# Performance work log

Measured on AMD Instinct MI355X. Metric: run time of the kernel, lower is better.

## Reference

```python
import jax, jax.numpy as jnp
import numpy as np

B, S, V, D, H, L = 2, 1024, 32000, 1024, 16, 4
DK = D // H
DF = 4 * D
EPS = 1e-5


def setup_inputs() -> dict:
    key = jax.random.key(0)
    ks = jax.random.split(key, 9)
    s = 0.02
    rn = lambda k, shape: jax.random.normal(k, shape, jnp.float32) * s
    return {
        "input_ids": jax.random.randint(ks[0], (B, S), 0, V, dtype=jnp.int32),
        "emb": rn(ks[1], (V, D)),
        "Wq": rn(ks[2], (L, D, D)),
        "Wk": rn(ks[3], (L, D, D)),
        "Wv": rn(ks[4], (L, D, D)),
        "Wo": rn(ks[5], (L, D, D)),
        "W1": rn(ks[6], (L, D, DF)),
        "b1": jnp.zeros((L, DF), jnp.float32),
        "W2": rn(ks[7], (L, DF, D)),
        "b2": jnp.zeros((L, D), jnp.float32),
        "ln1_g": jnp.ones((L, D), jnp.float32),
        "ln1_b": jnp.zeros((L, D), jnp.float32),
        "ln2_g": jnp.ones((L, D), jnp.float32),
        "ln2_b": jnp.zeros((L, D), jnp.float32),
        "lnf_g": jnp.ones((D,), jnp.float32),
        "lnf_b": jnp.zeros((D,), jnp.float32),
        "head_w": rn(ks[8], (D, V)),
    }


def _ln(x, g, b):
    m = jnp.mean(x, -1, keepdims=True)
    v = jnp.mean(jnp.square(x - m), -1, keepdims=True)
    return (x - m) * jax.lax.rsqrt(v + EPS) * g + b


def _heads(x):
    # [B,S,D] -> [B,H,S,DK]
    return x.reshape(B, S, H, DK).transpose(0, 2, 1, 3)


def _forward(input_ids, emb, Wq, Wk, Wv, Wo, W1, b1, W2, b2,
             ln1_g, ln1_b, ln2_g, ln2_b, lnf_g, lnf_b, head_w):
    x = emb[input_ids]  # [B,S,D]
    # causal mask: position q attends to k <= q (prefill, no past)
    mask = jnp.triu(jnp.full((S, S), -jnp.inf, jnp.float32), k=1)
    scale = 1.0 / np.sqrt(DK).astype(np.float32)

    def block(x, p):
        wq, wk, wv, wo, w1, bb1, w2, bb2, g1, be1, g2, be2 = p
        h = _ln(x, g1, be1)
        q = _heads(h @ wq)
        k = _heads(h @ wk)
        v = _heads(h @ wv)
        scores = jnp.einsum('bhqd,bhkd->bhqk', q, k) * scale + mask
        a = jax.nn.softmax(scores, axis=-1)
        o = jnp.einsum('bhqk,bhkd->bhqd', a, v)
        o = o.transpose(0, 2, 1, 3).reshape(B, S, D) @ wo
        x = x + o
        h2 = _ln(x, g2, be2)
        x = x + jax.nn.gelu(h2 @ w1 + bb1, approximate=False) @ w2 + bb2
        return x, None

    x, _ = jax.lax.scan(block, x, (Wq, Wk, Wv, Wo, W1, b1, W2, b2,
                                   ln1_g, ln1_b, ln2_g, ln2_b))
    logits = _ln(x, lnf_g, lnf_b) @ head_w  # [B,S,V]
    return logits


def reference(input_ids, emb, Wq, Wk, Wv, Wo, W1, b1, W2, b2,
              ln1_g, ln1_b, ln2_g, ln2_b, lnf_g, lnf_b, head_w):
    return _forward(input_ids, emb, Wq, Wk, Wv, Wo, W1, b1, W2, b2,
                    ln1_g, ln1_b, ln2_g, ln2_b, lnf_g, lnf_b, head_w)
```

## Files before the change

kernel.cpp:

```cpp
#include <hip/hip_runtime.h>
#include <stdint.h>

#define B_ 2
#define S_ 1024
#define V_ 32000
#define D_ 1024
#define H_ 16
#define L_ 4
#define DF_ 4096
#define M_ (B_*S_)

typedef short short8 __attribute__((ext_vector_type(8)));
typedef float f32x4 __attribute__((ext_vector_type(4)));

__device__ __forceinline__ unsigned short f2bf(float f){
  union { float f; unsigned int u; } v; v.f = f;
  unsigned int u = v.u;
  u = u + 0x7fffu + ((u >> 16) & 1u);
  return (unsigned short)(u >> 16);
}

__device__ __forceinline__ void gload16(const void* g, void* l){
  __builtin_amdgcn_global_load_lds(
      (__attribute__((address_space(1))) void*)(uintptr_t)g,
      (__attribute__((address_space(3))) void*)(uintptr_t)l, 16, 0, 0);
}

__global__ __launch_bounds__(256) void embed_k(const int* __restrict__ ids,
    const float* __restrict__ emb, float* __restrict__ x){
  int row = blockIdx.x;
  int id = ids[row];
  float4 v = reinterpret_cast<const float4*>(emb + (size_t)id*D_)[threadIdx.x];
  reinterpret_cast<float4*>(x + (size_t)row*D_)[threadIdx.x] = v;
}

__global__ __launch_bounds__(256) void ln_k(const float* __restrict__ x,
    const float* __restrict__ g, const float* __restrict__ b,
    unsigned short* __restrict__ out){
  int row = blockIdx.x;
  int tid = threadIdx.x;
  float4 v = reinterpret_cast<const float4*>(x + (size_t)row*D_)[tid];
  float s = v.x+v.y+v.z+v.w;
  float ss = v.x*v.x + v.y*v.y + v.z*v.z + v.w*v.w;
  #pragma unroll
  for (int off=1; off<64; off<<=1){ s += __shfl_xor(s, off); ss += __shfl_xor(ss, off); }
  __shared__ float rs[4], rss[4];
  int wave = tid>>6, lane = tid&63;
  if (lane==0){ rs[wave]=s; rss[wave]=ss; }
  __syncthreads();
  s  = rs[0]+rs[1]+rs[2]+rs[3];
  ss = rss[0]+rss[1]+rss[2]+rss[3];
  float mean = s * (1.0f/(float)D_);
  float var  = ss * (1.0f/(float)D_) - mean*mean;
  float inv = rsqrtf(var + 1e-5f);
  float4 gg = reinterpret_cast<const float4*>(g)[tid];
  float4 bb = reinterpret_cast<const float4*>(b)[tid];
  ushort4 o;
  o.x = f2bf((v.x-mean)*inv*gg.x + bb.x);
  o.y = f2bf((v.y-mean)*inv*gg.y + bb.y);
  o.z = f2bf((v.z-mean)*inv*gg.z + bb.z);
  o.w = f2bf((v.w-mean)*inv*gg.w + bb.w);
  reinterpret_cast<ushort4*>(out + (size_t)row*D_)[tid] = o;
}

__global__ __launch_bounds__(256) void rln_k(float* __restrict__ x,
    const float* __restrict__ part, const float* __restrict__ bias,
    const float* __restrict__ g, const float* __restrict__ b,
    unsigned short* __restrict__ out, int KS){
  int row = blockIdx.x;
  int tid = threadIdx.x;
  float4 v = reinterpret_cast<const float4*>(x + (size_t)row*D_)[tid];
  for (int z=0; z<KS; z++){
    float4 p = reinterpret_cast<const float4*>(part + (size_t)z*M_*D_ + (size_t)row*D_)[tid];
    v.x+=p.x; v.y+=p.y; v.z+=p.z; v.w+=p.w;
  }
  if (bias){
    float4 bb4 = reinterpret_cast<const float4*>(bias)[tid];
    v.x+=bb4.x; v.y+=bb4.y; v.z+=bb4.z; v.w+=bb4.w;
  }
  reinterpret_cast<float4*>(x + (size_t)row*D_)[tid] = v;
  float s = v.x+v.y+v.z+v.w;
  float ss = v.x*v.x + v.y*v.y + v.z*v.z + v.w*v.w;
  #pragma unroll
  for (int off=1; off<64; off<<=1){ s += __shfl_xor(s, off); ss += __shfl_xor(ss, off); }
  __shared__ float rs[4], rss[4];
  int wave = tid>>6, lane = tid&63;
  if (lane==0){ rs[wave]=s; rss[wave]=ss; }
  __syncthreads();
  s  = rs[0]+rs[1]+rs[2]+rs[3];
  ss = rss[0]+rss[1]+rss[2]+rss[3];
  float mean = s * (1.0f/(float)D_);
  float var  = ss * (1.0f/(float)D_) - mean*mean;
  float inv = rsqrtf(var + 1e-5f);
  float4 gg = reinterpret_cast<const float4*>(g)[tid];
  float4 bb = reinterpret_cast<const float4*>(b)[tid];
  ushort4 o;
  o.x = f2bf((v.x-mean)*inv*gg.x + bb.x);
  o.y = f2bf((v.y-mean)*inv*gg.y + bb.y);
  o.z = f2bf((v.z-mean)*inv*gg.z + bb.z);
  o.w = f2bf((v.w-mean)*inv*gg.w + bb.w);
  reinterpret_cast<ushort4*>(out + (size_t)row*D_)[tid] = o;
}

__global__ __launch_bounds__(256) void transpose_k(const float* __restrict__ in,
    unsigned short* __restrict__ out, int K, int N, size_t in_ls, size_t out_ls){
  __shared__ float t[64][65];
  const float* inp = in + (size_t)blockIdx.z*in_ls;
  unsigned short* outp = out + (size_t)blockIdx.z*out_ls;
  int k0 = blockIdx.y*64, n0 = blockIdx.x*64;
  int rr = threadIdx.x >> 4, c4 = (threadIdx.x & 15)*4;
  #pragma unroll
  for (int i=0;i<4;i++){
    float4 v = *reinterpret_cast<const float4*>(inp + (size_t)(k0+rr+i*16)*N + n0 + c4);
    t[rr+i*16][c4+0]=v.x; t[rr+i*16][c4+1]=v.y; t[rr+i*16][c4+2]=v.z; t[rr+i*16][c4+3]=v.w;
  }
  __syncthreads();
  #pragma unroll
  for (int i=0;i<4;i++){
    int n = rr + i*16;
    ushort4 o;
    o.x = f2bf(t[c4+0][n]); o.y = f2bf(t[c4+1][n]);
    o.z = f2bf(t[c4+2][n]); o.w = f2bf(t[c4+3][n]);
    *reinterpret_cast<ushort4*>(outp + (size_t)(n0+n)*K + k0 + c4) = o;
  }
}

template<int EP>
__global__ __launch_bounds__(256)
void gemm_bt(const unsigned short* __restrict__ A, const unsigned short* __restrict__ B,
             void* __restrict__ C, const float* __restrict__ bias,
             const float* __restrict__ resid, int K, int ldc, int MB, int kLen){
  __shared__ unsigned short As[2][128*64];
  __shared__ unsigned short Bs[2][128*64];
  const int tid = threadIdx.x;
  const int wave = tid>>6, lane = tid&63;
  const int wm = wave>>1, wn = wave&1;
  const int nwg = gridDim.x;
  const int p = blockIdx.x;
  const int t = (nwg & 7) ? p : ((p & 7)*(nwg>>3) + (p>>3));
  const int by = t % MB, bx = t / MB;
  const int row0 = by*128, col0 = bx*128;
  const int kz = blockIdx.z;
  const int k0 = kz*kLen;
  f32x4 acc[4][4] = {};
  const int sw8 = ((lane&7) ^ ((lane>>3)&7))*8;
  const unsigned short* Ag = A + (size_t)(row0 + wave*8 + (lane>>3))*K + sw8;
  const unsigned short* Bg = B + (size_t)(col0 + wave*8 + (lane>>3))*K + sw8;
  const int r = lane&15, g16 = lane>>4;
  const int rsw = (r&7)<<4;
#define STAGE_BT(buf, kt) do{ \
    _Pragma("unroll") \
    for (int i=0;i<4;i++){ \
      gload16(Ag + (size_t)i*32*K + (kt), As[buf] + (wave*8 + i*32)*64); \
      gload16(Bg + (size_t)i*32*K + (kt), Bs[buf] + (wave*8 + i*32)*64); \
    } }while(0)
  STAGE_BT(0, k0);
  __syncthreads();
  int cur = 0;
  for (int kt=k0; kt<k0+kLen; kt+=64){
    if (kt + 64 < k0 + kLen) STAGE_BT(cur^1, kt+64);
    #pragma unroll
    for (int ks=0; ks<2; ks++){
      short8 a[4], b[4];
      #pragma unroll
      for (int m=0;m<4;m++)
        a[m] = *reinterpret_cast<const short8*>((const char*)As[cur] + (wm*64+m*16+r)*128 + ((ks*64 + g16*16) ^ rsw));
      #pragma unroll
      for (int n=0;n<4;n++)
        b[n] = *reinterpret_cast<const short8*>((const char*)Bs[cur] + (wn*64+n*16+r)*128 + ((ks*64 + g16*16) ^ rsw));
      #pragma unroll
      for (int m=0;m<4;m++)
        #pragma unroll
        for (int n=0;n<4;n++)
          acc[m][n] = __builtin_amdgcn_mfma_f32_16x16x32_bf16(a[m], b[n], acc[m][n], 0,0,0);
    }
    __syncthreads();
    cur ^= 1;
  }
  float* Cp5 = (float*)C + (size_t)kz*M_*ldc;
  #pragma unroll
  for (int m=0;m<4;m++){
    const int row = row0 + wm*64 + m*16 + g16*4;
    #pragma unroll
    for (int n=0;n<4;n++){
      const int col = col0 + wn*64 + n*16 + r;
      #pragma unroll
      for (int j=0;j<4;j++){
        float val = acc[m][n][j];
        size_t idx = (size_t)(row+j)*ldc + col;
        if constexpr (EP==2 || EP==3) val += bias[col];
        if constexpr (EP==2) val = 0.5f*val*(1.0f + erff(val*0.70710678118f));
        if constexpr (EP==1 || EP==3) val += resid[idx];
        if constexpr (EP==0 || EP==2) ((unsigned short*)C)[idx] = f2bf(val);
        else if constexpr (EP==5) Cp5[idx] = val;
        else ((float*)C)[idx] = val;
      }
    }
  }
}

#define LDA8(buf,m,ks) (*(const short8*)(lds8 + (buf)*65536 + (wm*128+(m)*16+r)*128 + (((ks)*64+g16*16)^rsw)))
#define LDB8(buf,n,ks) (*(const short8*)(lds8 + (buf)*65536 + 32768 + (wn*64+(n)*16+r)*128 + (((ks)*64+g16*16)^rsw)))
#define STG(buf,isB,h,i,tile) gload16( \
    ((isB) ? Bw + (size_t)(col0 + (h)*128 + (i)*64 + wave*8 + srow)*K + (size_t)(tile)*64 + scsw \
           : A  + (size_t)(row0 + (h)*128 + (i)*64 + wave*8 + srow)*K + (size_t)(tile)*64 + scsw), \
    lds8 + (buf)*65536 + (isB)*32768 + ((h)*128 + (i)*64 + wave*8)*128 )
#define STG_HT(buf,isB,h,tile) do{ STG(buf,isB,h,0,tile); STG(buf,isB,h,1,tile); }while(0)
#define BLOAD8(bT) do{ \
  bfr[0][0]=LDB8(bT,0,0); bfr[0][1]=LDB8(bT,0,1); bfr[1][0]=LDB8(bT,1,0); bfr[1][1]=LDB8(bT,1,1); \
  bfr[2][0]=LDB8(bT,2,0); bfr[2][1]=LDB8(bT,2,1); bfr[3][0]=LDB8(bT,3,0); bfr[3][1]=LDB8(bT,3,1); }while(0)
#define MM8(mb,n) do{ \
  acc[mb][n]    =__builtin_amdgcn_mfma_f32_16x16x32_bf16(a0[0],bfr[n][0],acc[mb][n],0,0,0); \
  acc[mb][n]    =__builtin_amdgcn_mfma_f32_16x16x32_bf16(a0[1],bfr[n][1],acc[mb][n],0,0,0); \
  acc[(mb)+1][n]=__builtin_amdgcn_mfma_f32_16x16x32_bf16(a1[0],bfr[n][0],acc[(mb)+1][n],0,0,0); \
  acc[(mb)+1][n]=__builtin_amdgcn_mfma_f32_16x16x32_bf16(a1[1],bfr[n][1],acc[(mb)+1][n],0,0,0); }while(0)
#define VMC(n)  asm volatile("s_waitcnt vmcnt(" #n ")" ::: "memory")
#define PH8(bT, mb, STAGES, TAIL) do{ \
  short8 a0[2], a1[2]; \
  a0[0]=LDA8(bT,mb,0); a0[1]=LDA8(bT,mb,1); a1[0]=LDA8(bT,(mb)+1,0); a1[1]=LDA8(bT,(mb)+1,1); \
  STAGES; \
  __builtin_amdgcn_s_barrier(); \
  asm volatile("s_waitcnt lgkmcnt(0)" ::: "memory"); \
  __builtin_amdgcn_s_setprio(1); \
  MM8(mb,0); MM8(mb,1); MM8(mb,2); MM8(mb,3); \
  __builtin_amdgcn_s_setprio(0); \
  TAIL; \
  __builtin_amdgcn_s_barrier(); \
}while(0)

__global__ __launch_bounds__(512, 2)
void gemm_8ph(const unsigned short* __restrict__ A, const unsigned short* __restrict__ Bw,
              float* __restrict__ C, int K, int ldc, int MB){
  __shared__ char lds8[131072];
  const int tid = threadIdx.x;
  const int wave = tid>>6, lane = tid&63;
  const int wm = wave>>2, wn = wave&3;
  const int nwg = gridDim.x;
  const int pp = blockIdx.x;
  const int t = (nwg & 7) ? pp : ((pp & 7)*(nwg>>3) + (pp>>3));
  const int by = t % MB, bx = t / MB;
  const int row0 = by*256, col0 = bx*256;
  const int r = lane&15, g16 = lane>>4;
  const int rsw = (r&7)<<4;
  const int srow = lane>>3;
  const int scsw = ((lane&7) ^ srow)*8;

  f32x4 acc[8][4] = {};
  short8 bfr[4][2];
  const int NT = K/64;

  STG_HT(0,1,0,0); STG_HT(0,1,1,0);
  STG_HT(0,0,0,0); STG_HT(0,0,1,0);
  STG_HT(1,1,0,1); STG_HT(1,1,1,1);
  VMC(4);
  __builtin_amdgcn_s_barrier();

  for (int T0 = 0; T0 < NT-2; T0 += 2){
    BLOAD8(0);
    PH8(0, 0, STG_HT(1,0,0,T0+1), ((void)0));
    PH8(0, 2, STG_HT(1,0,1,T0+1), ((void)0));
    PH8(0, 4, STG_HT(0,1,0,T0+2), ((void)0));
    PH8(0, 6, STG_HT(0,1,1,T0+2), VMC(4));
    BLOAD8(1);
    PH8(1, 0, STG_HT(0,0,0,T0+2), ((void)0));
    PH8(1, 2, STG_HT(0,0,1,T0+2), ((void)0));
    PH8(1, 4, STG_HT(1,1,0,T0+3), ((void)0));
    PH8(1, 6, STG_HT(1,1,1,T0+3), VMC(4));
  }
  BLOAD8(0);
  PH8(0, 0, STG_HT(1,0,0,NT-1), ((void)0));
  PH8(0, 2, STG_HT(1,0,1,NT-1), ((void)0));
  PH8(0, 4, ((void)0), ((void)0));
  PH8(0, 6, ((void)0), VMC(0));
  BLOAD8(1);
  PH8(1, 0, ((void)0), ((void)0));
  PH8(1, 2, ((void)0), ((void)0));
  PH8(1, 4, ((void)0), ((void)0));
  PH8(1, 6, ((void)0), ((void)0));

  #pragma unroll
  for (int m=0;m<8;m++){
    const int row = row0 + wm*128 + m*16 + g16*4;
    #pragma unroll
    for (int n=0;n<4;n++){
      const int col = col0 + wn*64 + n*16 + r;
      #pragma unroll
      for (int j=0;j<4;j++)
        C[(size_t)(row+j)*ldc + col] = acc[m][n][j];
    }
  }
}

__global__ __launch_bounds__(256)
void attn_k(const unsigned short* __restrict__ qkv, unsigned short* __restrict__ o){
  __shared__ unsigned short Ks[64*64];
  __shared__ unsigned short Vt[64*64];
  __shared__ unsigned short Ps[4*16*64];
  const int tid = threadIdx.x;
  const int wave = tid>>6, lane = tid&63;
  const int qb = blockIdx.x, h = blockIdx.y, b = blockIdx.z;
  const int r = lane&15, g = lane>>4;
  const size_t rowbase = (size_t)b*S_*3*D_;
  short8 qf[2];
  {
    const unsigned short* qp = qkv + rowbase + (size_t)(qb*64 + wave*16 + r)*(3*D_) + h*64 + g*8;
    qf[0] = *reinterpret_cast<const short8*>(qp);
    qf[1] = *reinterpret_cast<const short8*>(qp + 32);
  }
  float mrow[4] = {-INFINITY,-INFINITY,-INFINITY,-INFINITY};
  float lrow[4] = {0.f,0.f,0.f,0.f};
  f32x4 oacc[4] = {};
  const int qglob0 = qb*64 + wave*16 + g*4;
  unsigned short* Pw = Ps + wave*16*64;

  for (int kt=0; kt<=qb; kt++){
    __syncthreads();
    #pragma unroll
    for (int i=0;i<2;i++){
      int key = i*32 + (tid>>3);
      int c8 = (tid&7)*8;
      const unsigned short* kp = qkv + rowbase + (size_t)(kt*64+key)*(3*D_) + D_ + h*64 + c8;
      uint4 kd = *reinterpret_cast<const uint4*>(kp);
      int bo = (key*128 + c8*2) ^ ((key&7)<<4);
      *reinterpret_cast<uint4*>((char*)Ks + bo) = kd;
      const unsigned short* vp = qkv + rowbase + (size_t)(kt*64+key)*(3*D_) + 2*D_ + h*64 + c8;
      uint4 vd = *reinterpret_cast<const uint4*>(vp);
      const unsigned short* ve = reinterpret_cast<const unsigned short*>(&vd);
      #pragma unroll
      for (int j=0;j<8;j++){
        int d = c8 + j;
        int bo2 = (d*128 + key*2) ^ ((d&7)<<4);
        *reinterpret_cast<unsigned short*>((char*)Vt + bo2) = ve[j];
      }
    }
    __syncthreads();
    f32x4 sacc[4] = {};
    #pragma unroll
    for (int ks=0; ks<2; ks++){
      #pragma unroll
      for (int nb=0; nb<4; nb++){
        int key = nb*16 + r;
        int bo = (key*128 + (ks*32+g*8)*2) ^ ((key&7)<<4);
        short8 kf = *reinterpret_cast<const short8*>((char*)Ks + bo);
        sacc[nb] = __builtin_amdgcn_mfma_f32_16x16x32_bf16(qf[ks], kf, sacc[nb], 0,0,0);
      }
    }
    float sv[4][4];
    float tm[4] = {-INFINITY,-INFINITY,-INFINITY,-INFINITY};
    #pragma unroll
    for (int nb=0; nb<4; nb++){
      int key = kt*64 + nb*16 + r;
      #pragma unroll
      for (int j=0;j<4;j++){
        float s = sacc[nb][j]*0.125f;
        s = (key <= qglob0 + j) ? s : -INFINITY;
        sv[nb][j] = s;
        tm[j] = fmaxf(tm[j], s);
      }
    }
    #pragma unroll
    for (int off=1; off<16; off<<=1){
      #pragma unroll
      for (int j=0;j<4;j++) tm[j] = fmaxf(tm[j], __shfl_xor(tm[j], off));
    }
    float sf[4], psum[4];
    #pragma unroll
    for (int j=0;j<4;j++){
      float mn = fmaxf(mrow[j], tm[j]);
      sf[j] = __expf(mrow[j]-mn);
      mrow[j] = mn;
      psum[j] = 0.0f;
    }
    #pragma unroll
    for (int nb=0; nb<4; nb++){
      #pragma unroll
      for (int j=0;j<4;j++){
        float p = __expf(sv[nb][j]-mrow[j]);
        psum[j] += p;
        int prow = g*4+j;
        int bo = (prow*128 + (nb*16+r)*2) ^ ((prow&7)<<4);
        *reinterpret_cast<unsigned short*>((char*)Pw + bo) = f2bf(p);
      }
    }
    #pragma unroll
    for (int off=1; off<16; off<<=1){
      #pragma unroll
      for (int j=0;j<4;j++) psum[j] += __shfl_xor(psum[j], off);
    }
    #pragma unroll
    for (int j=0;j<4;j++) lrow[j] = lrow[j]*sf[j] + psum[j];
    #pragma unroll
    for (int nb=0;nb<4;nb++){
      #pragma unroll
      for (int j=0;j<4;j++) oacc[nb][j] *= sf[j];
    }
    asm volatile("s_waitcnt lgkmcnt(0)" ::: "memory");
    #pragma unroll
    for (int ks=0; ks<2; ks++){
      int bo = (r*128 + (ks*32+g*8)*2) ^ ((r&7)<<4);
      short8 pf = *reinterpret_cast<const short8*>((char*)Pw + bo);
      #pragma unroll
      for (int nb=0; nb<4; nb++){
        int d = nb*16 + r;
        int bo2 = (d*128 + (ks*32+g*8)*2) ^ ((d&7)<<4);
        short8 vf = *reinterpret_cast<const short8*>((char*)Vt + bo2);
        oacc[nb] = __builtin_amdgcn_mfma_f32_16x16x32_bf16(pf, vf, oacc[nb], 0,0,0);
      }
    }
  }
  #pragma unroll
  for (int nb=0; nb<4; nb++){
    #pragma unroll
    for (int j=0;j<4;j++){
      float ov = oacc[nb][j] / lrow[j];
      size_t row = (size_t)b*S_ + qb*64 + wave*16 + g*4 + j;
      o[row*D_ + h*64 + nb*16 + r] = f2bf(ov);
    }
  }
}

extern "C" void kernel_launch(void* const* d_in, const int* in_sizes, int n_in,
                              void* d_out, int out_size, void* d_ws, size_t ws_size,
                              hipStream_t stream) {
  const int*   ids   = (const int*)  d_in[0];
  const float* emb   = (const float*)d_in[1];
  const float* Wq    = (const float*)d_in[2];
  const float* Wk    = (const float*)d_in[3];
  const float* Wv    = (const float*)d_in[4];
  const float* Wo    = (const float*)d_in[5];
  const float* W1    = (const float*)d_in[6];
  const float* b1    = (const float*)d_in[7];
  const float* W2    = (const float*)d_in[8];
  const float* b2    = (const float*)d_in[9];
  const float* ln1_g = (const float*)d_in[10];
  const float* ln1_b = (const float*)d_in[11];
  const float* ln2_g = (const float*)d_in[12];
  const float* ln2_b = (const float*)d_in[13];
  const float* lnf_g = (const float*)d_in[14];
  const float* lnf_b = (const float*)d_in[15];
  const float* headw = (const float*)d_in[16];

  unsigned short* ws = (unsigned short*)d_ws;
  unsigned short* wqkvT = ws;
  unsigned short* woT   = wqkvT + (size_t)L_*3*D_*D_;
  unsigned short* w1T   = woT   + (size_t)L_*D_*D_;
  unsigned short* w2T   = w1T   + (size_t)L_*D_*DF_;
  unsigned short* headT = w2T   + (size_t)L_*D_*DF_;
  unsigned short* h     = headT + (size_t)V_*D_;
  unsigned short* qkv   = h     + (size_t)M_*D_;
  unsigned short* attno = qkv   + (size_t)M_*3*D_;
  unsigned short* h2    = attno + (size_t)M_*D_;
  float*          x     = (float*)(h2 + (size_t)M_*DF_);
  float*          part  = x + (size_t)M_*D_;
  size_t needed = ((char*)(part + (size_t)2*M_*D_)) - (char*)d_ws;
  const bool splitk = (ws_size >= needed);

  transpose_k<<<dim3(D_/64, D_/64, L_), 256, 0, stream>>>(Wq, wqkvT,            D_, D_, (size_t)D_*D_, (size_t)3*D_*D_);
  transpose_k<<<dim3(D_/64, D_/64, L_), 256, 0, stream>>>(Wk, wqkvT + D_*D_,    D_, D_, (size_t)D_*D_, (size_t)3*D_*D_);
  transpose_k<<<dim3(D_/64, D_/64, L_), 256, 0, stream>>>(Wv, wqkvT + 2*D_*D_,  D_, D_, (size_t)D_*D_, (size_t)3*D_*D_);
  transpose_k<<<dim3(D_/64, D_/64, L_), 256, 0, stream>>>(Wo, woT,              D_, D_, (size_t)D_*D_, (size_t)D_*D_);
  transpose_k<<<dim3(DF_/64, D_/64, L_), 256, 0, stream>>>(W1, w1T,             D_, DF_, (size_t)D_*DF_, (size_t)D_*DF_);
  transpose_k<<<dim3(D_/64, DF_/64, L_), 256, 0, stream>>>(W2, w2T,             DF_, D_, (size_t)D_*DF_, (size_t)D_*DF_);
  transpose_k<<<dim3(V_/64, D_/64, 1), 256, 0, stream>>>(headw, headT,          D_, V_, 0, 0);

  embed_k<<<M_, 256, 0, stream>>>(ids, emb, x);
  ln_k<<<M_, 256, 0, stream>>>(x, ln1_g, ln1_b, h);

  for (int l = 0; l < L_; l++){
    gemm_bt<0><<<dim3((3*D_/128)*(M_/128), 1, 1), 256, 0, stream>>>(h, wqkvT + (size_t)l*3*D_*D_, qkv, nullptr, nullptr, D_, 3*D_, M_/128, D_);
    attn_k<<<dim3(S_/64, H_, B_), 256, 0, stream>>>(qkv, attno);
    if (splitk){
      gemm_bt<5><<<dim3((D_/128)*(M_/128), 1, 2), 256, 0, stream>>>(attno, woT + (size_t)l*D_*D_, part, nullptr, nullptr, D_, D_, M_/128, D_/2);
      rln_k<<<M_, 256, 0, stream>>>(x, part, nullptr, ln2_g + l*D_, ln2_b + l*D_, h, 2);
    } else {
      gemm_bt<1><<<dim3((D_/128)*(M_/128), 1, 1), 256, 0, stream>>>(attno, woT + (size_t)l*D_*D_, x, nullptr, x, D_, D_, M_/128, D_);
      ln_k<<<M_, 256, 0, stream>>>(x, ln2_g + l*D_, ln2_b + l*D_, h);
    }
    gemm_bt<2><<<dim3((DF_/128)*(M_/128), 1, 1), 256, 0, stream>>>(h, w1T + (size_t)l*D_*DF_, h2, b1 + l*DF_, nullptr, D_, DF_, M_/128, D_);
    const float* ng = (l+1 < L_) ? (ln1_g + (l+1)*D_) : lnf_g;
    const float* nb = (l+1 < L_) ? (ln1_b + (l+1)*D_) : lnf_b;
    if (splitk){
      gemm_bt<5><<<dim3((D_/128)*(M_/128), 1, 2), 256, 0, stream>>>(h2, w2T + (size_t)l*D_*DF_, part, nullptr, nullptr, DF_, D_, M_/128, DF_/2);
      rln_k<<<M_, 256, 0, stream>>>(x, part, b2 + l*D_, ng, nb, h, 2);
    } else {
      gemm_bt<3><<<dim3((D_/128)*(M_/128), 1, 1), 256, 0, stream>>>(h2, w2T + (size_t)l*D_*DF_, x, b2 + l*D_, x, DF_, D_, M_/128, DF_);
      ln_k<<<M_, 256, 0, stream>>>(x, ng, nb, h);
    }
  }

  gemm_8ph<<<dim3((V_/256)*(M_/256), 1, 1), 512, 0, stream>>>(h, headT, (float*)d_out, D_, V_, M_/256);
}
```

Baseline: 952.9 us.

## Use 8-wave phased 128x256 GEMM for layer matmuls with 4-way split-K

Adds a gemm_4ph kernel with 512 threads, a 128x256 tile, direct global-to-LDS loads, and an interleaved phase schedule where loads and MFMA run in alternating barriered phases. It replaces gemm_bt for the QKV, W1 (with GELU) and the split-K Wo/W2 GEMMs. Split-K for Wo/W2 goes from 2 to 4 slices, so the partial buffer doubles in size and rln_k sums 4 partials. The aim is better MFMA utilisation and load/compute overlap on the per-layer GEMMs. The cost is fewer workgroups for the QKV and W1 grids and more partial-sum traffic for the split-K GEMMs.

```diff
diff --git a/kernel.cpp b/kernel.cpp
--- a/kernel.cpp
+++ b/kernel.cpp
@@ -124,6 +124,8 @@
     *reinterpret_cast<ushort4*>(outp + (size_t)(n0+n)*K + k0 + c4) = o;
   }
 }
+
+#define VMC(n)  asm volatile("s_waitcnt vmcnt(" #n ")" ::: "memory")
 
 template<int EP>
 __global__ __launch_bounds__(256)
@@ -177,7 +179,6 @@
     __syncthreads();
     cur ^= 1;
   }
-  float* Cp5 = (float*)C + (size_t)kz*M_*ldc;
   #pragma unroll
   for (int m=0;m<4;m++){
     const int row = row0 + wm*64 + m*16 + g16*4;
@@ -192,7 +193,6 @@
         if constexpr (EP==2) val = 0.5f*val*(1.0f + erff(val*0.70710678118f));
         if constexpr (EP==1 || EP==3) val += resid[idx];
         if constexpr (EP==0 || EP==2) ((unsigned short*)C)[idx] = f2bf(val);
-        else if constexpr (EP==5) Cp5[idx] = val;
         else ((float*)C)[idx] = val;
       }
     }
@@ -214,7 +214,6 @@
   acc[mb][n]    =__builtin_amdgcn_mfma_f32_16x16x32_bf16(a0[1],bfr[n][1],acc[mb][n],0,0,0); \
   acc[(mb)+1][n]=__builtin_amdgcn_mfma_f32_16x16x32_bf16(a1[0],bfr[n][0],acc[(mb)+1][n],0,0,0); \
   acc[(mb)+1][n]=__builtin_amdgcn_mfma_f32_16x16x32_bf16(a1[1],bfr[n][1],acc[(mb)+1][n],0,0,0); }while(0)
-#define VMC(n)  asm volatile("s_waitcnt vmcnt(" #n ")" ::: "memory")
 #define PH8(bT, mb, STAGES, TAIL) do{ \
   short8 a0[2], a1[2]; \
   a0[0]=LDA8(bT,mb,0); a0[1]=LDA8(bT,mb,1); a1[0]=LDA8(bT,(mb)+1,0); a1[1]=LDA8(bT,(mb)+1,1); \
@@ -287,6 +286,101 @@
       #pragma unroll
       for (int j=0;j<4;j++)
         C[(size_t)(row+j)*ldc + col] = acc[m][n][j];
+    }
+  }
+}
+
+#define L4A(buf,m,ks) (*(const short8*)(lds4 + (buf)*49152 + (wm*64+(m)*16+r)*128 + (((ks)*64+g16*16)^rsw)))
+#define L4B(buf,n,ks) (*(const short8*)(lds4 + (buf)*49152 + 16384 + (wn*64+(n)*16+r)*128 + (((ks)*64+g16*16)^rsw)))
+#define STG4A(buf,tile) do{ \
+  gload16(A4 + (size_t)(row0 + 0*64 + wave*8 + srow)*K + (size_t)(tile)*64 + scsw, lds4 + (buf)*49152 + (0*64+wave*8)*128); \
+  gload16(A4 + (size_t)(row0 + 1*64 + wave*8 + srow)*K + (size_t)(tile)*64 + scsw, lds4 + (buf)*49152 + (1*64+wave*8)*128); }while(0)
+#define STG4B(buf,tile) do{ \
+  gload16(B4 + (size_t)(col0 + 0*64 + wave*8 + srow)*K + (size_t)(tile)*64 + scsw, lds4 + (buf)*49152 + 16384 + (0*64+wave*8)*128); \
+  gload16(B4 + (size_t)(col0 + 1*64 + wave*8 + srow)*K + (size_t)(tile)*64 + scsw, lds4 + (buf)*49152 + 16384 + (1*64+wave*8)*128); \
+  gload16(B4 + (size_t)(col0 + 2*64 + wave*8 + srow)*K + (size_t)(tile)*64 + scsw, lds4 + (buf)*49152 + 16384 + (2*64+wave*8)*128); \
+  gload16(B4 + (size_t)(col0 + 3*64 + wave*8 + srow)*K + (size_t)(tile)*64 + scsw, lds4 + (buf)*49152 + 16384 + (3*64+wave*8)*128); }while(0)
+#define BLOAD4(bT) do{ \
+  bfr4[0][0]=L4B(bT,0,0); bfr4[0][1]=L4B(bT,0,1); bfr4[1][0]=L4B(bT,1,0); bfr4[1][1]=L4B(bT,1,1); \
+  bfr4[2][0]=L4B(bT,2,0); bfr4[2][1]=L4B(bT,2,1); bfr4[3][0]=L4B(bT,3,0); bfr4[3][1]=L4B(bT,3,1); }while(0)
+#define MM44(mb,n) do{ \
+  acc[mb][n]    =__builtin_amdgcn_mfma_f32_16x16x32_bf16(a0[0],bfr4[n][0],acc[mb][n],0,0,0); \
+  acc[mb][n]    =__builtin_amdgcn_mfma_f32_16x16x32_bf16(a0[1],bfr4[n][1],acc[mb][n],0,0,0); \
+  acc[(mb)+1][n]=__builtin_amdgcn_mfma_f32_16x16x32_bf16(a1[0],bfr4[n][0],acc[(mb)+1][n],0,0,0); \
+  acc[(mb)+1][n]=__builtin_amdgcn_mfma_f32_16x16x32_bf16(a1[1],bfr4[n][1],acc[(mb)+1][n],0,0,0); }while(0)
+#define PH4(bT, mb, STAGES, TAIL) do{ \
+  short8 a0[2], a1[2]; \
+  a0[0]=L4A(bT,mb,0); a0[1]=L4A(bT,mb,1); a1[0]=L4A(bT,(mb)+1,0); a1[1]=L4A(bT,(mb)+1,1); \
+  STAGES; \
+  __builtin_amdgcn_s_barrier(); \
+  asm volatile("s_waitcnt lgkmcnt(0)" ::: "memory"); \
+  __builtin_amdgcn_s_setprio(1); \
+  MM44(mb,0); MM44(mb,1); MM44(mb,2); MM44(mb,3); \
+  __builtin_amdgcn_s_setprio(0); \
+  TAIL; \
+  __builtin_amdgcn_s_barrier(); \
+}while(0)
+
+template<int EP>
+__global__ __launch_bounds__(512, 2)
+void gemm_4ph(const unsigned short* __restrict__ A, const unsigned short* __restrict__ Bw,
+              void* __restrict__ C, const float* __restrict__ bias,
+              int K, int ldc, int MB, int kLen){
+  __shared__ char lds4[98304];
+  const int tid = threadIdx.x;
+  const int wave = tid>>6, lane = tid&63;
+  const int wm = wave>>2, wn = wave&3;
+  const int nwg = gridDim.x;
+  const int pp = blockIdx.x;
+  const int t = (nwg & 7) ? pp : ((pp & 7)*(nwg>>3) + (pp>>3));
+  const int by = t % MB, bx = t / MB;
+  const int row0 = by*128, col0 = bx*256;
+  const int r = lane&15, g16 = lane>>4;
+  const int rsw = (r&7)<<4;
+  const int srow = lane>>3;
+  const int scsw = ((lane&7) ^ srow)*8;
+  const int kz = blockIdx.z;
+  const unsigned short* A4 = A + (size_t)kz*kLen;
+  const unsigned short* B4 = Bw + (size_t)kz*kLen;
+
+  f32x4 acc[4][4] = {};
+  short8 bfr4[4][2];
+  const int NT = kLen/64;
+
+  STG4B(0,0); STG4A(0,0); STG4B(1,1);
+  VMC(4);
+  __builtin_amdgcn_s_barrier();
+
+  for (int T0 = 0; T0 < NT-2; T0 += 2){
+    BLOAD4(0);
+    PH4(0, 0, STG4A(1,T0+1), ((void)0));
+    PH4(0, 2, STG4B(0,T0+2), VMC(4));
+    BLOAD4(1);
+    PH4(1, 0, STG4A(0,T0+2), ((void)0));
+    PH4(1, 2, STG4B(1,T0+3), VMC(4));
+  }
+  BLOAD4(0);
+  PH4(0, 0, STG4A(1,NT-1), ((void)0));
+  PH4(0, 2, ((void)0), VMC(0));
+  BLOAD4(1);
+  PH4(1, 0, ((void)0), ((void)0));
+  PH4(1, 2, ((void)0), ((void)0));
+
+  float* Cp5 = (float*)C + (size_t)kz*M_*ldc;
+  #pragma unroll
+  for (int m=0;m<4;m++){
+    const int row = row0 + wm*64 + m*16 + g16*4;
+    #pragma unroll
+    for (int n=0;n<4;n++){
+      const int col = col0 + wn*64 + n*16 + r;
+      #pragma unroll
+      for (int j=0;j<4;j++){
+        float val = acc[m][n][j];
+        size_t idx = (size_t)(row+j)*ldc + col;
+        if constexpr (EP==2) { val += bias[col]; val = 0.5f*val*(1.0f + erff(val*0.70710678118f)); }
+        if constexpr (EP==0 || EP==2) ((unsigned short*)C)[idx] = f2bf(val);
+        else Cp5[idx] = val;
+      }
     }
   }
 }
@@ -452,7 +546,7 @@
   unsigned short* h2    = attno + (size_t)M_*D_;
   float*          x     = (float*)(h2 + (size_t)M_*DF_);
   float*          part  = x + (size_t)M_*D_;
-  size_t needed = ((char*)(part + (size_t)2*M_*D_)) - (char*)d_ws;
+  size_t needed = ((char*)(part + (size_t)4*M_*D_)) - (char*)d_ws;
   const bool splitk = (ws_size >= needed);
 
   transpose_k<<<dim3(D_/64, D_/64, L_), 256, 0, stream>>>(Wq, wqkvT,            D_, D_, (size_t)D_*D_, (size_t)3*D_*D_);
@@ -467,21 +561,21 @@
   ln_k<<<M_, 256, 0, stream>>>(x, ln1_g, ln1_b, h);
 
   for (int l = 0; l < L_; l++){
-    gemm_bt<0><<<dim3((3*D_/128)*(M_/128), 1, 1), 256, 0, stream>>>(h, wqkvT + (size_t)l*3*D_*D_, qkv, nullptr, nullptr, D_, 3*D_, M_/128, D_);
+    gemm_4ph<0><<<dim3((3*D_/256)*(M_/128), 1, 1), 512, 0, stream>>>(h, wqkvT + (size_t)l*3*D_*D_, qkv, nullptr, D_, 3*D_, M_/128, D_);
     attn_k<<<dim3(S_/64, H_, B_), 256, 0, stream>>>(qkv, attno);
     if (splitk){
-      gemm_bt<5><<<dim3((D_/128)*(M_/128), 1, 2), 256, 0, stream>>>(attno, woT + (size_t)l*D_*D_, part, nullptr, nullptr, D_, D_, M_/128, D_/2);
-      rln_k<<<M_, 256, 0, stream>>>(x, part, nullptr, ln2_g + l*D_, ln2_b + l*D_, h, 2);
+      gemm_4ph<5><<<dim3((D_/256)*(M_/128), 1, 4), 512, 0, stream>>>(attno, woT + (size_t)l*D_*D_, part, nullptr, D_, D_, M_/128, D_/4);
+      rln_k<<<M_, 256, 0, stream>>>(x, part, nullptr, ln2_g + l*D_, ln2_b + l*D_, h, 4);
     } else {
       gemm_bt<1><<<dim3((D_/128)*(M_/128), 1, 1), 256, 0, stream>>>(attno, woT + (size_t)l*D_*D_, x, nullptr, x, D_, D_, M_/128, D_);
       ln_k<<<M_, 256, 0, stream>>>(x, ln2_g + l*D_, ln2_b + l*D_, h);
     }
-    gemm_bt<2><<<dim3((DF_/128)*(M_/128), 1, 1), 256, 0, stream>>>(h, w1T + (size_t)l*D_*DF_, h2, b1 + l*DF_, nullptr, D_, DF_, M_/128, D_);
+    gemm_4ph<2><<<dim3((DF_/256)*(M_/128), 1, 1), 512, 0, stream>>>(h, w1T + (size_t)l*D_*DF_, h2, b1 + l*DF_, D_, DF_, M_/128, D_);
     const float* ng = (l+1 < L_) ? (ln1_g + (l+1)*D_) : lnf_g;
     const float* nb = (l+1 < L_) ? (ln1_b + (l+1)*D_) : lnf_b;
     if (splitk){
-      gemm_bt<5><<<dim3((D_/128)*(M_/128), 1, 2), 256, 0, stream>>>(h2, w2T + (size_t)l*D_*DF_, part, nullptr, nullptr, DF_, D_, M_/128, DF_/2);
-      rln_k<<<M_, 256, 0, stream>>>(x, part, b2 + l*D_, ng, nb, h, 2);
+      gemm_4ph<5><<<dim3((D_/256)*(M_/128), 1, 4), 512, 0, stream>>>(h2, w2T + (size_t)l*D_*DF_, part, nullptr, DF_, D_, M_/128, DF_/4);
+      rln_k<<<M_, 256, 0, stream>>>(x, part, b2 + l*D_, ng, nb, h, 4);
     } else {
       gemm_bt<3><<<dim3((D_/128)*(M_/128), 1, 1), 256, 0, stream>>>(h2, w2T + (size_t)l*D_*DF_, x, b2 + l*D_, x, DF_, D_, M_/128, DF_);
       ln_k<<<M_, 256, 0, stream>>>(x, ng, nb, h);
```

New measurement: 894.1 us. 6.2% less time.
